# Kernel tuning notes

Hardware: AMD Instinct MI355X
Metric: run time of the kernel (lower is better)

The kernel has to match this reference:

```python
import jax, jax.numpy as jnp
import numpy as np

B, S, H, E, V, OOV = 64, 400, 512, 256, 50000, 100

def setup_inputs() -> dict:
    key = jax.random.key(0)
    ks = jax.random.split(key, 32)
    p = lambda i, shape: jax.random.normal(ks[i], shape, jnp.float32) * 0.02
    emb = p(0, (V, E)).at[0].set(0.0)  # padding_idx=0
    return dict(
        summaries_in=jax.random.randint(ks[1], (B,), 1, V),
        h0=jax.random.normal(ks[2], (B, H), jnp.float32),
        c0=jax.random.normal(ks[3], (B, H), jnp.float32),
        encoder_out=jax.random.normal(ks[4], (B, S, 2 * H), jnp.float32),
        encoder_features=jax.random.normal(ks[5], (S * B, 2 * H), jnp.float32),
        encoder_mask=jnp.ones((S, B), jnp.float32),
        context=jax.random.normal(ks[6], (B, 2 * H), jnp.float32),
        coverage=jax.random.uniform(ks[7], (S, B), jnp.float32) * 0.01,
        texts_extended=jax.random.randint(ks[8], (S, B), 0, V + OOV),
        oov_size=OOV,
        emb=emb,
        W_feat=p(10, (2 * H, 2 * H)), b_feat=p(11, (2 * H,)),
        W_cov=p(12, (2 * H,)), b_cov=p(13, (2 * H,)),
        w_att=p(14, (2 * H,)), b_att=p(15, ()),
        W_ih=p(16, (4 * H, E)), W_hh=p(17, (4 * H, H)),
        b_ih=p(18, (4 * H,)), b_hh=p(19, (4 * H,)),
        W_ctx=p(20, (E, 2 * H + E)), b_ctx=p(21, (E,)),
        W_pg=p(22, (4 * H + E,)), b_pg=p(23, ()),
        W_o1=p(24, (H, 3 * H)), b_o1=p(25, (H,)),
        W_o2=p(26, (V, H)), b_o2=p(27, (V,)),
    )


def reference(summaries_in, h0, c0, encoder_out, encoder_features, encoder_mask,
              context, coverage, texts_extended, oov_size, emb,
              W_feat, b_feat, W_cov, b_cov, w_att, b_att,
              W_ih, W_hh, b_ih, b_hh, W_ctx, b_ctx, W_pg, b_pg,
              W_o1, b_o1, W_o2, b_o2):
    # embedding + context projection: [B, 2H+E] -> [B, E]
    x = emb[summaries_in]
    ctx_out = jnp.concatenate([context, x], axis=1) @ W_ctx.T + b_ctx
    # single LSTM step (torch gate order i, f, g, o)
    gates = ctx_out @ W_ih.T + b_ih + h0 @ W_hh.T + b_hh
    i, f, g, o = jnp.split(gates, 4, axis=1)
    c = jax.nn.sigmoid(f) * c0 + jax.nn.sigmoid(i) * jnp.tanh(g)
    h = jax.nn.sigmoid(o) * jnp.tanh(c)
    hidden_out = jnp.concatenate([h, c], axis=1)  # [B, 2H]
    # Bahdanau attention with coverage
    dec_feat = hidden_out @ W_feat.T + b_feat                 # [B, 2H]
    ef = encoder_features.reshape(S, B, 2 * H)                # [S, B, 2H]
    cov_feat = coverage[..., None] * W_cov + b_cov            # Linear(1, 2H)
    e = jnp.tanh(ef + dec_feat[None] + cov_feat) @ w_att + b_att  # [S, B]
    a = jax.nn.softmax(e, axis=0) * encoder_mask
    a = a / jnp.sum(a, axis=0, keepdims=True)                 # renormalize (Normalize(0))
    ctx_new = jnp.einsum('sb,bsd->bd', a, encoder_out)        # [B, 2H]
    coverage_next = coverage + a
    # pointer-generator mix
    gen_in = jnp.concatenate([ctx_new, hidden_out, ctx_out], axis=1)  # [B, 4H+E]
    p_gen = jax.nn.sigmoid(gen_in @ W_pg + b_pg)[:, None]             # [B, 1]
    logits = (jnp.concatenate([h, ctx_new], axis=1) @ W_o1.T + b_o1) @ W_o2.T + b_o2
    vocab_dist = p_gen * jax.nn.softmax(logits, axis=1)       # [B, V]
    attn_w = (1.0 - p_gen) * a.T                              # [B, S]
    vd = jnp.concatenate([vocab_dist, jnp.zeros((B, oov_size), vocab_dist.dtype)], axis=1)
    vd = vd.at[jnp.arange(B)[:, None], texts_extended.T].add(attn_w)  # scatter_add copy dist
    return vd, hidden_out, ctx_new, a, coverage_next
```

## Files before the change

kernel.cpp:

```cpp
#include <hip/hip_runtime.h>
#include <cmath>

#define B 64
#define S 400
#define H 512
#define E 256
#define V 50000
#define OOV 100
#define H2 1024
#define VDN (V + OOV)
#define NBLK_V 782
#define SC 40

typedef __attribute__((ext_vector_type(8))) short short8;
typedef __attribute__((ext_vector_type(4))) float f32x4;

__device__ __forceinline__ float wred_sum(float v) {
#pragma unroll
  for (int o = 32; o > 0; o >>= 1) v += __shfl_down(v, o, 64);
  return v;
}
__device__ __forceinline__ float wred_max(float v) {
#pragma unroll
  for (int o = 32; o > 0; o >>= 1) v = fmaxf(v, __shfl_down(v, o, 64));
  return v;
}
__device__ __forceinline__ short f2bf(float f) {
  return __builtin_bit_cast(short, (__bf16)f);
}
__device__ __forceinline__ float ftanh(float x) {
  float e = __expf(2.f * x);
  return 1.f - 2.f * __builtin_amdgcn_rcpf(e + 1.f);
}
__device__ __forceinline__ float fsig(float x) {
  return __builtin_amdgcn_rcpf(1.f + __expf(-x));
}

__global__ __launch_bounds__(256) void k_pre(
    const float* __restrict__ b_ctx, const float* __restrict__ b_ih,
    const float* __restrict__ b_hh, const float* __restrict__ b_feat,
    const float* __restrict__ b_o1, const float* __restrict__ context,
    const float* __restrict__ emb, const int* __restrict__ sumin,
    const float* __restrict__ h0, float* __restrict__ ctxoutT4,
    float* __restrict__ gates, float* __restrict__ dfeat,
    float* __restrict__ innerT4, float* __restrict__ catT4,
    float* __restrict__ h0T4) {
  int idx = blockIdx.x * 256 + threadIdx.x;
  if (idx < 16384) {
    int j = ((idx >> 8) << 2) + (idx & 3);
    ctxoutT4[idx] = b_ctx[j];
  } else if (idx < 16384 + 131072) {
    int i = idx - 16384;
    int j = i & 2047;
    gates[i] = b_ih[j] + b_hh[j];
  } else if (idx < 16384 + 131072 + 65536) {
    int i = idx - 16384 - 131072;
    dfeat[i] = b_feat[i & 1023];
  } else if (idx < 245760) {
    int i = idx - 16384 - 131072 - 65536;
    int j = ((i >> 8) << 2) + (i & 3);
    innerT4[i] = b_o1[j];
  } else if (idx < 245760 + 81920) {
    int i = idx - 245760;
    int e = i & 3, b = (i >> 2) & 63, q = i >> 8;
    int k = q * 4 + e;
    catT4[i] = (k < 1024) ? context[b * 1024 + k]
                          : emb[(size_t)sumin[b] * 256 + (k - 1024)];
  } else {
    int i = idx - 245760 - 81920;
    int e = i & 3, b = (i >> 2) & 63, q = i >> 8;
    h0T4[i] = h0[b * 512 + q * 4 + e];
  }
}

template <int R, int KC, int OUTMODE>
__global__ __launch_bounds__(256) void k_gemmsk(
    const float* __restrict__ A1, const float* __restrict__ W1, int ldw1, int s1,
    const float* __restrict__ A2, const float* __restrict__ W2, int ldw2,
    float* __restrict__ out, int ldout) {
  const int lane = threadIdx.x;
  const int w = threadIdx.y;
  const int j0 = blockIdx.x * (4 * R) + w * R;
  const float* A;
  const float* W;
  int ldw, kc0;
  if ((int)blockIdx.y < s1) {
    A = A1; W = W1; ldw = ldw1; kc0 = blockIdx.y * KC;
  } else {
    A = A2; W = W2; ldw = ldw2; kc0 = (blockIdx.y - s1) * KC;
  }
  float acc[R];
#pragma unroll
  for (int r = 0; r < R; ++r) acc[r] = 0.f;
  const float* ap = A + (size_t)kc0 * 256 + lane * 4;
  const float* wr[R];
#pragma unroll
  for (int r = 0; r < R; ++r) wr[r] = W + (size_t)(j0 + r) * ldw + kc0 * 4;
#pragma unroll 8
  for (int k4 = 0; k4 < KC; ++k4) {
    float4 av = *(const float4*)(ap + (size_t)k4 * 256);
#pragma unroll
    for (int r = 0; r < R; ++r) {
      float4 wv = *(const float4*)(wr[r] + k4 * 4);
      acc[r] += av.x * wv.x + av.y * wv.y + av.z * wv.z + av.w * wv.w;
    }
  }
#pragma unroll
  for (int r = 0; r < R; ++r) {
    int j = j0 + r;
    if constexpr (OUTMODE == 0)
      atomicAdd(&out[((size_t)(j >> 2) * 64 + lane) * 4 + (j & 3)], acc[r]);
    else
      atomicAdd(&out[(size_t)lane * ldout + j], acc[r]);
  }
}

__global__ __launch_bounds__(256) void k_lstm(const float* __restrict__ gates,
                                              const float* __restrict__ c0,
                                              float* __restrict__ hidden,
                                              float* __restrict__ hcT4) {
  int idx = blockIdx.x * 256 + threadIdx.x;
  int b = idx >> 9, u = idx & 511;
  float gi = gates[(size_t)b * 2048 + u];
  float gf = gates[(size_t)b * 2048 + 512 + u];
  float gg = gates[(size_t)b * 2048 + 1024 + u];
  float go = gates[(size_t)b * 2048 + 1536 + u];
  float c = fsig(gf) * c0[(size_t)b * 512 + u] + fsig(gi) * ftanh(gg);
  float h = fsig(go) * ftanh(c);
  hidden[(size_t)b * H2 + u] = h;
  hidden[(size_t)b * H2 + 512 + u] = c;
  hcT4[((u >> 2) * 64 + b) * 4 + (u & 3)] = h;
  int k = 512 + u;
  hcT4[((k >> 2) * 64 + b) * 4 + (k & 3)] = c;
}

__global__ __launch_bounds__(256) void k_e(
    const float* __restrict__ ef, const float* __restrict__ dfeat,
    const float* __restrict__ cov, const float* __restrict__ Wcov,
    const float* __restrict__ bcov, const float* __restrict__ watt,
    const float* __restrict__ batt, float* __restrict__ e_out) {
  const int t = threadIdx.x;
  const int b = blockIdx.x & 63;
  const int q = blockIdx.x >> 6;
  float4 dv = ((const float4*)(dfeat + (size_t)b * H2))[t];
  float4 bc = ((const float4*)bcov)[t];
  float4 wc = ((const float4*)Wcov)[t];
  float4 wa = ((const float4*)watt)[t];
  const float bx = dv.x + bc.x, by = dv.y + bc.y;
  const float bz = dv.z + bc.z, bw = dv.w + bc.w;
  __shared__ float part[8][5];
#pragma unroll
  for (int i = 0; i < 8; ++i) {
    const int s = q * 8 + i;
    const int sb = s * B + b;
    const float cval = cov[sb];
    float4 ev = ((const float4*)(ef + (size_t)sb * H2))[t];
    float sum = ftanh(ev.x + bx + cval * wc.x) * wa.x +
                ftanh(ev.y + by + cval * wc.y) * wa.y +
                ftanh(ev.z + bz + cval * wc.z) * wa.z +
                ftanh(ev.w + bw + cval * wc.w) * wa.w;
    sum = wred_sum(sum);
    if ((t & 63) == 0) part[i][t >> 6] = sum;
  }
  __syncthreads();
  if (t < 8) {
    e_out[(q * 8 + t) * B + b] =
        part[t][0] + part[t][1] + part[t][2] + part[t][3] + batt[0];
  }
}

__global__ __launch_bounds__(512) void k_soft(const float* __restrict__ e,
                                              const float* __restrict__ mask,
                                              const float* __restrict__ cov_in,
                                              float* __restrict__ a_out,
                                              float* __restrict__ cov_out) {
  const int b = blockIdx.x;
  const int s = threadIdx.x;
  __shared__ float red[8];
  float ev = (s < S) ? e[s * B + b] : -INFINITY;
  float m = wred_max(ev);
  if ((s & 63) == 0) red[s >> 6] = m;
  __syncthreads();
  if (s == 0) {
    float mm = red[0];
#pragma unroll
    for (int i = 1; i < 8; ++i) mm = fmaxf(mm, red[i]);
    red[0] = mm;
  }
  __syncthreads();
  m = red[0];
  float ex = (s < S) ? mask[s * B + b] * __expf(ev - m) : 0.f;
  float ws = wred_sum(ex);
  __syncthreads();
  if ((s & 63) == 0) red[s >> 6] = ws;
  __syncthreads();
  if (s == 0) {
    float z = 0.f;
#pragma unroll
    for (int i = 0; i < 8; ++i) z += red[i];
    red[0] = z;
  }
  __syncthreads();
  float Z = red[0];
  if (s < S) {
    float av = ex / Z;
    a_out[s * B + b] = av;
    cov_out[s * B + b] = cov_in[s * B + b] + av;
  }
}

__global__ __launch_bounds__(256) void k_ctxp(const float* __restrict__ a,
                                              const float* __restrict__ enc,
                                              float* __restrict__ part) {
  const int b = blockIdx.x & 63;
  const int sc = blockIdx.x >> 6;
  const int d = threadIdx.x * 4;
  float4 acc = make_float4(0.f, 0.f, 0.f, 0.f);
#pragma unroll
  for (int i = 0; i < 10; ++i) {
    int s = sc * 10 + i;
    float av = a[s * B + b];
    float4 ev = *(const float4*)(enc + ((size_t)b * S + s) * H2 + d);
    acc.x += av * ev.x;
    acc.y += av * ev.y;
    acc.z += av * ev.z;
    acc.w += av * ev.w;
  }
  *(float4*)(part + (size_t)blockIdx.x * H2 + d) = acc;
}

__global__ __launch_bounds__(256) void k_ctxred(const float* __restrict__ part,
                                                float* __restrict__ ctx_new,
                                                float* __restrict__ ctxT4) {
  int idx = blockIdx.x * 256 + threadIdx.x;
  float s = 0.f;
#pragma unroll
  for (int sc = 0; sc < SC; ++sc) s += part[(size_t)sc * 65536 + idx];
  int b = idx >> 10, d = idx & 1023;
  ctx_new[idx] = s;
  ctxT4[((d >> 2) * 64 + b) * 4 + (d & 3)] = s;
}

__global__ __launch_bounds__(256) void k_pgen(
    const float* __restrict__ ctx_new, const float* __restrict__ hidden,
    const float* __restrict__ ctxoutT4, const float* __restrict__ Wpg,
    const float* __restrict__ bpg, float* __restrict__ pgen) {
  const int b = blockIdx.x;
  float p = 0.f;
  for (int k = threadIdx.x; k < 2304; k += 256) {
    float v;
    if (k < 1024) v = ctx_new[(size_t)b * H2 + k];
    else if (k < 2048) v = hidden[(size_t)b * H2 + k - 1024];
    else {
      int ko = k - 2048;
      v = ctxoutT4[((ko >> 2) * 64 + b) * 4 + (ko & 3)];
    }
    p += v * Wpg[k];
  }
  p = wred_sum(p);
  __shared__ float red[4];
  if ((threadIdx.x & 63) == 0) red[threadIdx.x >> 6] = p;
  __syncthreads();
  if (threadIdx.x == 0) {
    float d = red[0] + red[1] + red[2] + red[3] + bpg[0];
    pgen[b] = fsig(d);
  }
}

__global__ __launch_bounds__(256) void k_packinner(const float* __restrict__ innerT4,
                                                   short8* __restrict__ packB) {
  int f = blockIdx.x * 256 + threadIdx.x;
  int l = f & 63, bt = (f >> 6) & 3, ks = f >> 8;
  int b = bt * 16 + (l & 15);
  int kbase = ks * 32 + (l >> 4) * 8;
  float4 q0 = *(const float4*)&innerT4[(size_t)(kbase / 4) * 256 + b * 4];
  float4 q1 = *(const float4*)&innerT4[(size_t)(kbase / 4 + 1) * 256 + b * 4];
  short8 frag;
  frag[0] = f2bf(q0.x); frag[1] = f2bf(q0.y);
  frag[2] = f2bf(q0.z); frag[3] = f2bf(q0.w);
  frag[4] = f2bf(q1.x); frag[5] = f2bf(q1.y);
  frag[6] = f2bf(q1.z); frag[7] = f2bf(q1.w);
  packB[f] = frag;
}

__global__ __launch_bounds__(256) void k_mfma_logits(
    const float* __restrict__ W2, const short8* __restrict__ packB,
    const float* __restrict__ bias, float* __restrict__ logits,
    float* __restrict__ mp, float* __restrict__ zp) {
  const int l = threadIdx.x;
  const int w = threadIdx.y;
  const int jblk = blockIdx.x * 64;
  const int jw = jblk + w * 16;
  const int jv = min(jw + (l & 15), V - 1);
  const float4* wp4 = (const float4*)(W2 + (size_t)jv * 512 + (l >> 4) * 8);

  f32x4 acc0 = {0.f, 0.f, 0.f, 0.f}, acc1 = acc0, acc2 = acc0, acc3 = acc0;
  float4 cw0 = wp4[0], cw1 = wp4[1];
#pragma unroll
  for (int ks = 0; ks < 16; ++ks) {
    float4 nw0, nw1;
    if (ks < 15) { nw0 = wp4[(ks + 1) * 8]; nw1 = wp4[(ks + 1) * 8 + 1]; }
    short8 af;
    af[0] = f2bf(cw0.x); af[1] = f2bf(cw0.y); af[2] = f2bf(cw0.z); af[3] = f2bf(cw0.w);
    af[4] = f2bf(cw1.x); af[5] = f2bf(cw1.y); af[6] = f2bf(cw1.z); af[7] = f2bf(cw1.w);
    short8 b0 = packB[(ks * 4 + 0) * 64 + l];
    short8 b1 = packB[(ks * 4 + 1) * 64 + l];
    short8 b2 = packB[(ks * 4 + 2) * 64 + l];
    short8 b3 = packB[(ks * 4 + 3) * 64 + l];
    acc0 = __builtin_amdgcn_mfma_f32_16x16x32_bf16(af, b0, acc0, 0, 0, 0);
    acc1 = __builtin_amdgcn_mfma_f32_16x16x32_bf16(af, b1, acc1, 0, 0, 0);
    acc2 = __builtin_amdgcn_mfma_f32_16x16x32_bf16(af, b2, acc2, 0, 0, 0);
    acc3 = __builtin_amdgcn_mfma_f32_16x16x32_bf16(af, b3, acc3, 0, 0, 0);
    if (ks < 15) { cw0 = nw0; cw1 = nw1; }
  }

  __shared__ float tile[64][65];
  const int rbase = w * 16 + (l >> 4) * 4;
#pragma unroll
  for (int v = 0; v < 4; ++v) {
    int jl = rbase + v;
    int j = jblk + jl;
    float bv = bias[min(j, V - 1)];
    bool valid = (j < V);
    tile[jl][0 * 16 + (l & 15)] = valid ? acc0[v] + bv : -INFINITY;
    tile[jl][1 * 16 + (l & 15)] = valid ? acc1[v] + bv : -INFINITY;
    tile[jl][2 * 16 + (l & 15)] = valid ? acc2[v] + bv : -INFINITY;
    tile[jl][3 * 16 + (l & 15)] = valid ? acc3[v] + bv : -INFINITY;
  }
  __syncthreads();
  const int t = w * 64 + l;
#pragma unroll
  for (int i = 0; i < 16; ++i) {
    int idx = i * 256 + t;
    int jl = idx & 63;
    int b = idx >> 6;
    int j = jblk + jl;
    if (j < V) logits[(size_t)b * V + j] = tile[jl][b];
  }
  if (t < 64) {
    float m = -INFINITY;
#pragma unroll
    for (int jl = 0; jl < 64; ++jl) m = fmaxf(m, tile[jl][t]);
    float z = 0.f;
#pragma unroll
    for (int jl = 0; jl < 64; ++jl) z += __expf(tile[jl][t] - m);
    mp[(size_t)blockIdx.x * 64 + t] = m;
    zp[(size_t)blockIdx.x * 64 + t] = z;
  }
}

__global__ __launch_bounds__(256) void k_vdm(const float* __restrict__ logits,
                                             const float* __restrict__ mp,
                                             const float* __restrict__ zp,
                                             const float* __restrict__ pgen,
                                             float* __restrict__ out) {
  const int b = blockIdx.x >> 3;
  const int c = blockIdx.x & 7;
  const int t = threadIdx.x;
  __shared__ float red[4];
  float m = -INFINITY;
  for (int i = t; i < NBLK_V; i += 256) m = fmaxf(m, mp[i * 64 + b]);
  m = wred_max(m);
  if ((t & 63) == 0) red[t >> 6] = m;
  __syncthreads();
  const float M = fmaxf(fmaxf(red[0], red[1]), fmaxf(red[2], red[3]));
  float z = 0.f;
  for (int i = t; i < NBLK_V; i += 256) z += zp[i * 64 + b] * __expf(mp[i * 64 + b] - M);
  z = wred_sum(z);
  __syncthreads();
  if ((t & 63) == 0) red[t >> 6] = z;
  __syncthreads();
  const float Z = red[0] + red[1] + red[2] + red[3];
  const float scale = pgen[b] / Z;
  const int v0 = c * 6272;
  const int v1 = min(v0 + 6272, VDN);
  for (int v = v0 + t; v < v1; v += 256) {
    float val = (v < V) ? scale * __expf(logits[(size_t)b * V + v] - M) : 0.f;
    out[(size_t)b * VDN + v] = val;
  }
}

__global__ __launch_bounds__(256) void k_scatter(const float* __restrict__ a,
                                                 const int* __restrict__ tex,
                                                 const float* __restrict__ pgen,
                                                 float* __restrict__ vd) {
  int g = blockIdx.x * 256 + threadIdx.x;
  if (g >= S * B) return;
  int b = g & 63;
  float w = (1.f - pgen[b]) * a[g];
  atomicAdd(&vd[(size_t)b * VDN + tex[g]], w);
}

extern "C" void kernel_launch(void* const* d_in, const int* in_sizes, int n_in,
                              void* d_out, int out_size, void* d_ws, size_t ws_size,
                              hipStream_t stream) {
  const int* sumin = (const int*)d_in[0];
  const float* h0 = (const float*)d_in[1];
  const float* c0 = (const float*)d_in[2];
  const float* enc_out = (const float*)d_in[3];
  const float* ef = (const float*)d_in[4];
  const float* mask = (const float*)d_in[5];
  const float* context = (const float*)d_in[6];
  const float* coverage = (const float*)d_in[7];
  const int* tex = (const int*)d_in[8];
  const float* emb = (const float*)d_in[10];
  const float* W_feat = (const float*)d_in[11];
  const float* b_feat = (const float*)d_in[12];
  const float* W_cov = (const float*)d_in[13];
  const float* b_cov = (const float*)d_in[14];
  const float* w_att = (const float*)d_in[15];
  const float* b_att = (const float*)d_in[16];
  const float* W_ih = (const float*)d_in[17];
  const float* W_hh = (const float*)d_in[18];
  const float* b_ih = (const float*)d_in[19];
  const float* b_hh = (const float*)d_in[20];
  const float* W_ctx = (const float*)d_in[21];
  const float* b_ctx = (const float*)d_in[22];
  const float* W_pg = (const float*)d_in[23];
  const float* b_pg = (const float*)d_in[24];
  const float* W_o1 = (const float*)d_in[25];
  const float* b_o1 = (const float*)d_in[26];
  const float* W_o2 = (const float*)d_in[27];
  const float* b_o2 = (const float*)d_in[28];

  float* out = (float*)d_out;
  float* vd = out;
  float* hidden = vd + (size_t)B * VDN;
  float* ctx_new = hidden + (size_t)B * H2;
  float* a_out = ctx_new + (size_t)B * H2;
  float* cov_out = a_out + (size_t)S * B;

  float* ws = (float*)d_ws;
  float* catT4 = ws;
  float* h0T4 = catT4 + 81920;
  float* ctxoutT4 = h0T4 + 32768;
  float* gates = ctxoutT4 + 16384;
  float* hidcatT4 = gates + 131072;
  float* dfeat = hidcatT4 + 65536;
  float* e_ws = dfeat + 65536;
  float* ctxnewT4 = e_ws + 25600;
  float* innerT4 = ctxnewT4 + 65536;
  float* pgen = innerT4 + 32768;
  float* mp = pgen + 64;
  float* zp = mp + 50048;
  float* packBf = zp + 50048;
  float* logits = packBf + 16384;
  float* part = logits;
  short8* packB = (short8*)packBf;

  dim3 gblk(64, 4);

  k_pre<<<1408, 256, 0, stream>>>(b_ctx, b_ih, b_hh, b_feat, b_o1, context, emb,
                                  sumin, h0, ctxoutT4, gates, dfeat, innerT4,
                                  catT4, h0T4);
  k_gemmsk<2, 64, 0><<<dim3(32, 5), gblk, 0, stream>>>(
      catT4, W_ctx, 1280, 5, nullptr, nullptr, 0, ctxoutT4, 0);
  k_gemmsk<2, 64, 1><<<dim3(256, 3), gblk, 0, stream>>>(
      ctxoutT4, W_ih, 256, 1, h0T4, W_hh, 512, gates, 2048);
  k_lstm<<<128, 256, 0, stream>>>(gates, c0, hidden, hidcatT4);
  k_gemmsk<2, 64, 1><<<dim3(128, 4), gblk, 0, stream>>>(
      hidcatT4, W_feat, 1024, 4, nullptr, nullptr, 0, dfeat, 1024);
  k_e<<<50 * 64, 256, 0, stream>>>(ef, dfeat, coverage, W_cov, b_cov, w_att,
                                   b_att, e_ws);
  k_soft<<<B, 512, 0, stream>>>(e_ws, mask, coverage, a_out, cov_out);
  k_ctxp<<<SC * B, 256, 0, stream>>>(a_out, enc_out, part);
  k_ctxred<<<256, 256, 0, stream>>>(part, ctx_new, ctxnewT4);
  k_pgen<<<B, 256, 0, stream>>>(ctx_new, hidden, ctxoutT4, W_pg, b_pg, pgen);
  k_gemmsk<2, 64, 0><<<dim3(64, 6), gblk, 0, stream>>>(
      hidcatT4, W_o1, 1536, 2, ctxnewT4, W_o1 + 512, 1536, innerT4, 0);
  k_packinner<<<16, 256, 0, stream>>>(innerT4, packB);
  k_mfma_logits<<<NBLK_V, gblk, 0, stream>>>(W_o2, packB, b_o2, logits, mp, zp);
  k_vdm<<<B * 8, 256, 0, stream>>>(logits, mp, zp, pgen, vd);
  k_scatter<<<100, 256, 0, stream>>>(a_out, tex, pgen, vd);
}
```

Before: 216.5 us.

## Fuse softmax into context partials, merge ctx reduction with p_gen, fold scatter into vocab

Each context-partial block now recomputes the attention softmax max and sum for its batch column instead of relying on a separate softmax kernel. The number of sequence chunks drops from 40 to 8, so partials shrink and the reduction is fused with the p_gen dot product. The copy-distribution scatter moves into the vocab-distribution kernel as a shared-memory histogram per vocab chunk, which removes the global atomics and a launch. The cost is redundant softmax work in every block, a 25KB LDS allocation in the vocab kernel, and fewer blocks for the context partials.

```diff
diff --git a/kernel.cpp b/kernel.cpp
--- a/kernel.cpp
+++ b/kernel.cpp
@@ -10,7 +10,7 @@
 #define H2 1024
 #define VDN (V + OOV)
 #define NBLK_V 782
-#define SC 40
+#define SC 8
 
 typedef __attribute__((ext_vector_type(8))) short short8;
 typedef __attribute__((ext_vector_type(4))) float f32x4;
@@ -169,57 +169,46 @@
   }
 }
 
-__global__ __launch_bounds__(512) void k_soft(const float* __restrict__ e,
-                                              const float* __restrict__ mask,
-                                              const float* __restrict__ cov_in,
-                                              float* __restrict__ a_out,
-                                              float* __restrict__ cov_out) {
-  const int b = blockIdx.x;
-  const int s = threadIdx.x;
-  __shared__ float red[8];
-  float ev = (s < S) ? e[s * B + b] : -INFINITY;
-  float m = wred_max(ev);
-  if ((s & 63) == 0) red[s >> 6] = m;
-  __syncthreads();
-  if (s == 0) {
-    float mm = red[0];
-#pragma unroll
-    for (int i = 1; i < 8; ++i) mm = fmaxf(mm, red[i]);
-    red[0] = mm;
-  }
-  __syncthreads();
-  m = red[0];
-  float ex = (s < S) ? mask[s * B + b] * __expf(ev - m) : 0.f;
-  float ws = wred_sum(ex);
-  __syncthreads();
-  if ((s & 63) == 0) red[s >> 6] = ws;
-  __syncthreads();
-  if (s == 0) {
-    float z = 0.f;
-#pragma unroll
-    for (int i = 0; i < 8; ++i) z += red[i];
-    red[0] = z;
-  }
-  __syncthreads();
-  float Z = red[0];
-  if (s < S) {
-    float av = ex / Z;
-    a_out[s * B + b] = av;
-    cov_out[s * B + b] = cov_in[s * B + b] + av;
-  }
-}
-
-__global__ __launch_bounds__(256) void k_ctxp(const float* __restrict__ a,
-                                              const float* __restrict__ enc,
-                                              float* __restrict__ part) {
+__global__ __launch_bounds__(256) void k_softctx(
+    const float* __restrict__ e_ws, const float* __restrict__ mask,
+    const float* __restrict__ coverage, const float* __restrict__ enc,
+    float* __restrict__ a_out, float* __restrict__ cov_out,
+    float* __restrict__ part) {
   const int b = blockIdx.x & 63;
   const int sc = blockIdx.x >> 6;
-  const int d = threadIdx.x * 4;
+  const int t = threadIdx.x;
+  const int lane = t & 63, w = t >> 6;
+  __shared__ float red[4];
+  __shared__ float aS[50];
+  float e1 = e_ws[t * B + b];
+  float e2 = (t < S - 256) ? e_ws[(t + 256) * B + b] : -INFINITY;
+  float m = wred_max(fmaxf(e1, e2));
+  if (lane == 0) red[w] = m;
+  __syncthreads();
+  const float M = fmaxf(fmaxf(red[0], red[1]), fmaxf(red[2], red[3]));
+  __syncthreads();
+  float x1 = mask[t * B + b] * __expf(e1 - M);
+  float x2 = (t < S - 256) ? mask[(t + 256) * B + b] * __expf(e2 - M) : 0.f;
+  float zs = wred_sum(x1 + x2);
+  if (lane == 0) red[w] = zs;
+  __syncthreads();
+  const float Z = red[0] + red[1] + red[2] + red[3];
+  const float rZ = 1.f / Z;
+  if (t < 50) {
+    int s = sc * 50 + t;
+    float ex = mask[s * B + b] * __expf(e_ws[s * B + b] - M);
+    float av = ex * rZ;
+    aS[t] = av;
+    a_out[s * B + b] = av;
+    cov_out[s * B + b] = coverage[s * B + b] + av;
+  }
+  __syncthreads();
+  const int d = t * 4;
   float4 acc = make_float4(0.f, 0.f, 0.f, 0.f);
-#pragma unroll
-  for (int i = 0; i < 10; ++i) {
-    int s = sc * 10 + i;
-    float av = a[s * B + b];
+#pragma unroll 10
+  for (int i = 0; i < 50; ++i) {
+    int s = sc * 50 + i;
+    float av = aS[i];
     float4 ev = *(const float4*)(enc + ((size_t)b * S + s) * H2 + d);
     acc.x += av * ev.x;
     acc.y += av * ev.y;
@@ -229,41 +218,37 @@
   *(float4*)(part + (size_t)blockIdx.x * H2 + d) = acc;
 }
 
-__global__ __launch_bounds__(256) void k_ctxred(const float* __restrict__ part,
-                                                float* __restrict__ ctx_new,
-                                                float* __restrict__ ctxT4) {
-  int idx = blockIdx.x * 256 + threadIdx.x;
-  float s = 0.f;
-#pragma unroll
-  for (int sc = 0; sc < SC; ++sc) s += part[(size_t)sc * 65536 + idx];
-  int b = idx >> 10, d = idx & 1023;
-  ctx_new[idx] = s;
-  ctxT4[((d >> 2) * 64 + b) * 4 + (d & 3)] = s;
-}
-
-__global__ __launch_bounds__(256) void k_pgen(
-    const float* __restrict__ ctx_new, const float* __restrict__ hidden,
+__global__ __launch_bounds__(256) void k_ctxpg(
+    const float* __restrict__ part, const float* __restrict__ hidden,
     const float* __restrict__ ctxoutT4, const float* __restrict__ Wpg,
-    const float* __restrict__ bpg, float* __restrict__ pgen) {
+    const float* __restrict__ bpg, float* __restrict__ ctx_new,
+    float* __restrict__ ctxT4, float* __restrict__ pgen) {
   const int b = blockIdx.x;
-  float p = 0.f;
-  for (int k = threadIdx.x; k < 2304; k += 256) {
-    float v;
-    if (k < 1024) v = ctx_new[(size_t)b * H2 + k];
-    else if (k < 2048) v = hidden[(size_t)b * H2 + k - 1024];
-    else {
-      int ko = k - 2048;
-      v = ctxoutT4[((ko >> 2) * 64 + b) * 4 + (ko & 3)];
-    }
-    p += v * Wpg[k];
-  }
+  const int t = threadIdx.x;
+  const int lane = t & 63, w = t >> 6;
+  const int d = t * 4;
+  float4 s = make_float4(0.f, 0.f, 0.f, 0.f);
+#pragma unroll
+  for (int sc = 0; sc < SC; ++sc) {
+    float4 v = *(const float4*)(part + (size_t)(sc * 64 + b) * H2 + d);
+    s.x += v.x; s.y += v.y; s.z += v.z; s.w += v.w;
+  }
+  *(float4*)(ctx_new + (size_t)b * H2 + d) = s;
+  *(float4*)(ctxT4 + (size_t)t * 256 + b * 4) = s;
+  float p = s.x * Wpg[d] + s.y * Wpg[d + 1] + s.z * Wpg[d + 2] + s.w * Wpg[d + 3];
+#pragma unroll
+  for (int j = 0; j < 4; ++j) {
+    int k = t + j * 256;
+    p += hidden[(size_t)b * H2 + k] * Wpg[1024 + k];
+  }
+  p += ctxoutT4[(size_t)(t >> 2) * 256 + b * 4 + (t & 3)] * Wpg[2048 + t];
   p = wred_sum(p);
   __shared__ float red[4];
-  if ((threadIdx.x & 63) == 0) red[threadIdx.x >> 6] = p;
-  __syncthreads();
-  if (threadIdx.x == 0) {
-    float d = red[0] + red[1] + red[2] + red[3] + bpg[0];
-    pgen[b] = fsig(d);
+  if (lane == 0) red[w] = p;
+  __syncthreads();
+  if (t == 0) {
+    float dd = red[0] + red[1] + red[2] + red[3] + bpg[0];
+    pgen[b] = fsig(dd);
   }
 }
 
@@ -290,8 +275,7 @@
   const int l = threadIdx.x;
   const int w = threadIdx.y;
   const int jblk = blockIdx.x * 64;
-  const int jw = jblk + w * 16;
-  const int jv = min(jw + (l & 15), V - 1);
+  const int jv = min(jblk + w * 16 + (l & 15), V - 1);
   const float4* wp4 = (const float4*)(W2 + (size_t)jv * 512 + (l >> 4) * 8);
 
   f32x4 acc0 = {0.f, 0.f, 0.f, 0.f}, acc1 = acc0, acc2 = acc0, acc3 = acc0;
@@ -349,46 +333,46 @@
   }
 }
 
-__global__ __launch_bounds__(256) void k_vdm(const float* __restrict__ logits,
-                                             const float* __restrict__ mp,
-                                             const float* __restrict__ zp,
-                                             const float* __restrict__ pgen,
-                                             float* __restrict__ out) {
+__global__ __launch_bounds__(256) void k_vdms(
+    const float* __restrict__ logits, const float* __restrict__ mp,
+    const float* __restrict__ zp, const float* __restrict__ pgen,
+    const float* __restrict__ a_out, const int* __restrict__ tex,
+    float* __restrict__ out) {
   const int b = blockIdx.x >> 3;
   const int c = blockIdx.x & 7;
   const int t = threadIdx.x;
+  const int lane = t & 63, w = t >> 6;
   __shared__ float red[4];
+  __shared__ float hist[6272];
   float m = -INFINITY;
   for (int i = t; i < NBLK_V; i += 256) m = fmaxf(m, mp[i * 64 + b]);
   m = wred_max(m);
-  if ((t & 63) == 0) red[t >> 6] = m;
+  if (lane == 0) red[w] = m;
   __syncthreads();
   const float M = fmaxf(fmaxf(red[0], red[1]), fmaxf(red[2], red[3]));
+  __syncthreads();
   float z = 0.f;
   for (int i = t; i < NBLK_V; i += 256) z += zp[i * 64 + b] * __expf(mp[i * 64 + b] - M);
   z = wred_sum(z);
-  __syncthreads();
-  if ((t & 63) == 0) red[t >> 6] = z;
+  if (lane == 0) red[w] = z;
   __syncthreads();
   const float Z = red[0] + red[1] + red[2] + red[3];
-  const float scale = pgen[b] / Z;
+  const float pg = pgen[b];
+  const float scale = pg / Z;
+  const float wq = 1.f - pg;
   const int v0 = c * 6272;
   const int v1 = min(v0 + 6272, VDN);
+  for (int i = t; i < 6272; i += 256) hist[i] = 0.f;
+  __syncthreads();
+  for (int s = t; s < S; s += 256) {
+    int v = tex[s * B + b];
+    if (v >= v0 && v < v1) atomicAdd(&hist[v - v0], wq * a_out[s * B + b]);
+  }
+  __syncthreads();
   for (int v = v0 + t; v < v1; v += 256) {
     float val = (v < V) ? scale * __expf(logits[(size_t)b * V + v] - M) : 0.f;
-    out[(size_t)b * VDN + v] = val;
-  }
-}
-
-__global__ __launch_bounds__(256) void k_scatter(const float* __restrict__ a,
-                                                 const int* __restrict__ tex,
-                                                 const float* __restrict__ pgen,
-                                                 float* __restrict__ vd) {
-  int g = blockIdx.x * 256 + threadIdx.x;
-  if (g >= S * B) return;
-  int b = g & 63;
-  float w = (1.f - pgen[b]) * a[g];
-  atomicAdd(&vd[(size_t)b * VDN + tex[g]], w);
+    out[(size_t)b * VDN + v] = val + hist[v - v0];
+  }
 }
 
 extern "C" void kernel_launch(void* const* d_in, const int* in_sizes, int n_in,
@@ -462,14 +446,13 @@
       hidcatT4, W_feat, 1024, 4, nullptr, nullptr, 0, dfeat, 1024);
   k_e<<<50 * 64, 256, 0, stream>>>(ef, dfeat, coverage, W_cov, b_cov, w_att,
                                    b_att, e_ws);
-  k_soft<<<B, 512, 0, stream>>>(e_ws, mask, coverage, a_out, cov_out);
-  k_ctxp<<<SC * B, 256, 0, stream>>>(a_out, enc_out, part);
-  k_ctxred<<<256, 256, 0, stream>>>(part, ctx_new, ctxnewT4);
-  k_pgen<<<B, 256, 0, stream>>>(ctx_new, hidden, ctxoutT4, W_pg, b_pg, pgen);
+  k_softctx<<<SC * B, 256, 0, stream>>>(e_ws, mask, coverage, enc_out, a_out,
+                                        cov_out, part);
+  k_ctxpg<<<B, 256, 0, stream>>>(part, hidden, ctxoutT4, W_pg, b_pg, ctx_new,
+                                 ctxnewT4, pgen);
   k_gemmsk<2, 64, 0><<<dim3(64, 6), gblk, 0, stream>>>(
       hidcatT4, W_o1, 1536, 2, ctxnewT4, W_o1 + 512, 1536, innerT4, 0);
   k_packinner<<<16, 256, 0, stream>>>(innerT4, packB);
   k_mfma_logits<<<NBLK_V, gblk, 0, stream>>>(W_o2, packB, b_o2, logits, mp, zp);
-  k_vdm<<<B * 8, 256, 0, stream>>>(logits, mp, zp, pgen, vd);
-  k_scatter<<<100, 256, 0, stream>>>(a_out, tex, pgen, vd);
-}
+  k_vdms<<<B * 8, 256, 0, stream>>>(logits, mp, zp, pgen, a_out, tex, vd);
+}
```

New measurement: 206.5 us. -4.6%, faster.
